# Kernel optimization log

Measured on AMD Instinct MI355X. Metric: run time of the kernel, lower is better.

The kernel has to match this reference:

```python
import jax, jax.numpy as jnp
import numpy as np

H, W = 256, 256
N_PIXELS = H * W
MAX_DIST = float(np.sqrt(H ** 2 + W ** 2))
RESIZED = jnp.array([H, W], dtype=jnp.float32)

# all_img_locations: cartesian product of rows x cols, shape [N_PIXELS, 2] as (row, col)
_rr, _cc = jnp.meshgrid(jnp.arange(H), jnp.arange(W), indexing='ij')
LOCS = jnp.stack([_rr, _cc], axis=-1).reshape(-1, 2).astype(jnp.float32)


def setup_inputs() -> dict:
    key = jax.random.key(0)
    k1, k2, k3 = jax.random.split(key, 3)
    B, M = 8, 128
    # probability map in open interval (0,1) so log(p) and log(1-p) are finite
    prob_map = jnp.clip(jax.random.uniform(k1, (B, H, W), dtype=jnp.float32), 1e-4, 1.0 - 1e-4)
    # gt heatmap: mostly <1 with a sprinkling of exact 1.0 'center' pixels (so pos_count > 0)
    u = jax.random.uniform(k2, (B, H, W), dtype=jnp.float32)
    gt_map = jnp.where(u > 0.999, jnp.float32(1.0), u * 0.999)
    # ground-truth points (row, col) in [0, H) x [0, W)
    gt = jax.random.uniform(k3, (B, M, 2), dtype=jnp.float32) * RESIZED
    # original image sizes (height, width)
    orig_sizes = jnp.ones((B, 2), dtype=jnp.float32) * 1024.0
    return {"prob_map": prob_map, "gt_map": gt_map, "gt": gt, "orig_sizes": orig_sizes}


def _center_focal_loss(pred, g, alpha=2, beta=4):
    pos = (g == 1.0).astype(pred.dtype)
    neg = (g < 1.0).astype(pred.dtype)
    pos_term = (1.0 - pred) ** alpha * jnp.log(pred) * pos
    neg_term = (1.0 - g) ** beta * pred ** alpha * jnp.log1p(-pred) * neg
    return -((pos_term + neg_term).sum() / pos.sum())


def _whd_terms(pm_b, gt_b, orig_size_b):
    norm = orig_size_b / RESIZED                      # [2]
    nx = LOCS * norm                                  # [N, 2]
    ny = gt_b * norm                                  # [M, 2]
    diff = nx[:, None, :] - ny[None, :, :]            # [N, M, 2]
    d = jnp.sqrt(jnp.sum(diff * diff, axis=-1))       # [N, M]
    p = pm_b.reshape(-1)                              # [N]
    n_est = p.sum()
    term1 = jnp.sum(p * d.min(axis=1)) / (n_est + 1e-6)
    weighted = (1.0 - p)[:, None] * MAX_DIST + p[:, None] * d
    term2 = weighted.min(axis=0).mean()               # generalized mean reduces to min over pixels
    return term1, term2


def reference(prob_map, gt_map, gt, orig_sizes):
    terms_1, terms_2 = jax.vmap(_whd_terms)(prob_map, gt, orig_sizes)
    # original loop overwrites terms_3 each iteration -> only last batch element's focal loss survives
    terms_3 = _center_focal_loss(prob_map[-1], gt_map[-1])
    return terms_1.mean() + terms_2.mean() + terms_3
```

## Files before the change

### kernel.cpp

```cpp
#include <hip/hip_runtime.h>
#include <math.h>


#define HH 256
#define WW 256
#define NPIX (HH*WW)
#define MM 128
#define BB 8
#define MAXDIST 362.03867196751236f
#define PBLK 128
#define NBLK (BB*PBLK)
#define TPB 256
#define PXT 2
#define MCH 16
#define NCH (MM/MCH)
#define POISON 0xAAAAAAAAu
#define LASTTOK (POISON + (unsigned)(NBLK - 1))

__device__ __forceinline__ float fast_sqrt(float x) {
  float r;
  asm volatile("v_sqrt_f32 %0, %1" : "=v"(r) : "v"(x));
  return r;
}

__device__ __forceinline__ float wave_sum(float v) {
#pragma unroll
  for (int off = 32; off > 0; off >>= 1) v += __shfl_xor(v, off, 64);
  return v;
}

__global__ __launch_bounds__(TPB, 4) void whd_fused(
    const float* __restrict__ prob, const float* __restrict__ gtmap,
    const float* __restrict__ gt, const float* __restrict__ osz,
    unsigned* __restrict__ colmin,
    float* __restrict__ partials,
    unsigned* __restrict__ counter,
    float* __restrict__ out) {
  const int b   = blockIdx.x >> 7;
  const int blk = blockIdx.x & (PBLK - 1);
  const int tid = threadIdx.x;
  const int lane = tid & 63;

  __shared__ float2 sgt[MM];
  __shared__ float wred[TPB / 64][4];
  __shared__ int lastFlag;
  __shared__ float sT[TPB / 64];
  __shared__ float sA[BB], sC[BB], sF[BB], sG[BB];

  const float ny = osz[b * 2 + 0] * (1.0f / HH);
  const float nx = osz[b * 2 + 1] * (1.0f / WW);

  if (tid < MM) {
    float gy = gt[(b * MM + tid) * 2 + 0] * ny;
    float gx = gt[(b * MM + tid) * 2 + 1] * nx;
    sgt[tid] = make_float2(gy, gx);
  }
  __syncthreads();

  const int pixBase = blk * (NPIX / PBLK) + tid * PXT;
  const float pyf = (float)(pixBase >> 8) * ny;
  const int col0 = pixBase & (WW - 1);

  const float* pp = prob + b * NPIX + pixBase;
  float2 pv = *(const float2*)(pp);
  float p[PXT] = {pv.x, pv.y};

  float pxf[PXT], bb[PXT], md[PXT];
#pragma unroll
  for (int i = 0; i < PXT; i++) {
    pxf[i] = (float)(col0 + i) * nx;
    bb[i]  = (1.0f - p[i]) * MAXDIST;
    md[i]  = 3.0e38f;
  }

#pragma unroll 1
  for (int c = 0; c < NCH; c++) {
    float gx[MCH], dy2[MCH], cm[MCH];
#pragma unroll
    for (int j = 0; j < MCH; j++) {
      float2 g = sgt[c * MCH + j];
      float dy = pyf - g.x;
      dy2[j] = dy * dy;
      gx[j]  = g.y;
      cm[j]  = 3.0e38f;
    }
#pragma unroll
    for (int i = 0; i < PXT; i++) {
      const float pi = p[i], bi = bb[i], xi = pxf[i];
      float mdi = md[i];
#pragma unroll
      for (int j = 0; j < MCH; j++) {
        float dx = xi - gx[j];
        float d  = fast_sqrt(fmaf(dx, dx, dy2[j]));
        mdi   = fminf(mdi, d);
        cm[j] = fminf(cm[j], fmaf(pi, d, bi));
      }
      md[i] = mdi;
    }

    {
      const bool hi5 = (lane & 32) != 0;
#pragma unroll
      for (int k = 0; k < 8; k++) {
        float keep = hi5 ? cm[k + 8] : cm[k];
        float send = hi5 ? cm[k] : cm[k + 8];
        cm[k] = fminf(keep, __shfl_xor(send, 32, 64));
      }
      const bool hi4 = (lane & 16) != 0;
#pragma unroll
      for (int k = 0; k < 4; k++) {
        float keep = hi4 ? cm[k + 4] : cm[k];
        float send = hi4 ? cm[k] : cm[k + 4];
        cm[k] = fminf(keep, __shfl_xor(send, 16, 64));
      }
      const bool hi3 = (lane & 8) != 0;
#pragma unroll
      for (int k = 0; k < 2; k++) {
        float keep = hi3 ? cm[k + 2] : cm[k];
        float send = hi3 ? cm[k] : cm[k + 2];
        cm[k] = fminf(keep, __shfl_xor(send, 8, 64));
      }
      const bool hi2 = (lane & 4) != 0;
      {
        float keep = hi2 ? cm[1] : cm[0];
        float send = hi2 ? cm[0] : cm[1];
        cm[0] = fminf(keep, __shfl_xor(send, 4, 64));
      }
      float v = cm[0];
      v = fminf(v, __shfl_xor(v, 1, 64));
      v = fminf(v, __shfl_xor(v, 2, 64));
      if ((lane & 3) == 0)
        atomicMin(&colmin[b * MM + c * MCH + (lane >> 2)], __float_as_uint(v));
    }
  }

  float spd = 0.0f, sp = 0.0f;
#pragma unroll
  for (int i = 0; i < PXT; i++) {
    spd = fmaf(p[i], md[i], spd);
    sp += p[i];
  }

  float fs = 0.0f, fc = 0.0f;
  if (b == BB - 1) {
    const float* gp = gtmap + b * NPIX + pixBase;
    float2 gv2 = *(const float2*)(gp);
    float gv[PXT] = {gv2.x, gv2.y};
#pragma unroll
    for (int i = 0; i < PXT; i++) {
      float g = gv[i], pi = p[i];
      if (g == 1.0f) {
        float om = 1.0f - pi;
        fs += om * om * logf(pi);
        fc += 1.0f;
      } else {
        float t = 1.0f - g, t2 = t * t;
        fs += t2 * t2 * pi * pi * log1pf(-pi);
      }
    }
  }

  spd = wave_sum(spd);
  sp  = wave_sum(sp);
  fs  = wave_sum(fs);
  fc  = wave_sum(fc);

  const int wid = tid >> 6;
  if (lane == 0) {
    wred[wid][0] = spd; wred[wid][1] = sp; wred[wid][2] = fs; wred[wid][3] = fc;
  }
  __syncthreads();

  if (tid == 0) {
    float a = 0, c2 = 0, e = 0, f = 0;
#pragma unroll
    for (int w = 0; w < TPB / 64; w++) {
      a += wred[w][0]; c2 += wred[w][1]; e += wred[w][2]; f += wred[w][3];
    }
    float* pt = partials + blockIdx.x * 4;
    pt[0] = a; pt[1] = c2; pt[2] = e; pt[3] = f;
    __threadfence();
    unsigned old = atomicAdd(counter, 1u);
    lastFlag = (old == LASTTOK) ? 1 : 0;
  }
  __syncthreads();
  if (lastFlag == 0) return;

  __threadfence();

  float s = 0.0f;
  for (int i = tid; i < BB * MM; i += TPB)
    s += __uint_as_float(atomicAdd(&colmin[i], 0u));
  s = wave_sum(s);
  if (lane == 0) sT[wid] = s;

  const int g = tid >> 5;
  const int i = tid & 31;
  float a = 0, c = 0, e = 0, f = 0;
  for (int k = i; k < PBLK; k += 32) {
    float* pt = partials + (g * PBLK + k) * 4;
    a += atomicAdd(pt + 0, 0.0f);
    c += atomicAdd(pt + 1, 0.0f);
    e += atomicAdd(pt + 2, 0.0f);
    f += atomicAdd(pt + 3, 0.0f);
  }
#pragma unroll
  for (int off = 16; off > 0; off >>= 1) {
    a += __shfl_xor(a, off, 64); c += __shfl_xor(c, off, 64);
    e += __shfl_xor(e, off, 64); f += __shfl_xor(f, off, 64);
  }
  if (i == 0) { sA[g] = a; sC[g] = c; sF[g] = e; sG[g] = f; }
  __syncthreads();

  if (tid == 0) {
    float t2 = (sT[0] + sT[1] + sT[2] + sT[3]) * (1.0f / (BB * MM));
    float t1 = 0.0f;
    for (int b2 = 0; b2 < BB; b2++) t1 += sA[b2] / (sC[b2] + 1e-6f);
    t1 *= (1.0f / BB);
    float fsum = 0.0f, fcnt = 0.0f;
    for (int b2 = 0; b2 < BB; b2++) { fsum += sF[b2]; fcnt += sG[b2]; }
    out[0] = t1 + t2 - fsum / fcnt;
  }
}

extern "C" void kernel_launch(void* const* d_in, const int* in_sizes, int n_in,
                              void* d_out, int out_size, void* d_ws, size_t ws_size,
                              hipStream_t stream) {
  const float* prob  = (const float*)d_in[0];
  const float* gtmap = (const float*)d_in[1];
  const float* gt    = (const float*)d_in[2];
  const float* osz   = (const float*)d_in[3];
  float* out = (float*)d_out;

  unsigned* colmin  = (unsigned*)d_ws;
  float* partials   = (float*)((char*)d_ws + 4096);
  unsigned* counter = (unsigned*)((char*)d_ws + 4096 + NBLK * 16);

  whd_fused<<<NBLK, TPB, 0, stream>>>(prob, gtmap, gt, osz, colmin, partials,
                                      counter, out);
}
```

Measured before the change: 98.93 us.

## Partition GT points across waves and stage pixels through LDS to cut shuffles and atomics

Each wave now owns 32 of the 128 GT points for the whole run and loops over all 512 pixels of the block, which are staged in shared memory. Column minima stay in registers across all pixel groups, so the butterfly shuffle reduction and the atomicMin to global happen once per block instead of once per 16-point chunk. Per-pixel row minima are combined across waves through a shared-memory buffer. The sqrt asm also loses `volatile` so the compiler is free to schedule it. The cost is more registers for the 32-entry arrays, about 10 KB of extra LDS, and an extra barrier.

```diff
diff --git a/kernel.cpp b/kernel.cpp
--- a/kernel.cpp
+++ b/kernel.cpp
@@ -11,15 +11,15 @@
 #define PBLK 128
 #define NBLK (BB*PBLK)
 #define TPB 256
-#define PXT 2
-#define MCH 16
-#define NCH (MM/MCH)
+#define NW 4
+#define MW 32
+#define PIXB 512
 #define POISON 0xAAAAAAAAu
 #define LASTTOK (POISON + (unsigned)(NBLK - 1))
 
 __device__ __forceinline__ float fast_sqrt(float x) {
   float r;
-  asm volatile("v_sqrt_f32 %0, %1" : "=v"(r) : "v"(x));
+  asm("v_sqrt_f32 %0, %1" : "=v"(r) : "v"(x));
   return r;
 }
 
@@ -36,16 +36,20 @@
     float* __restrict__ partials,
     unsigned* __restrict__ counter,
     float* __restrict__ out) {
-  const int b   = blockIdx.x >> 7;
-  const int blk = blockIdx.x & (PBLK - 1);
-  const int tid = threadIdx.x;
+  const int b    = blockIdx.x >> 7;
+  const int blk  = blockIdx.x & (PBLK - 1);
+  const int tid  = threadIdx.x;
   const int lane = tid & 63;
+  const int w    = tid >> 6;
 
   __shared__ float2 sgt[MM];
-  __shared__ float wred[TPB / 64][4];
-  __shared__ int lastFlag;
-  __shared__ float sT[TPB / 64];
-  __shared__ float sA[BB], sC[BB], sF[BB], sG[BB];
+  __shared__ float  sp[PIXB];
+  __shared__ float  mdw[NW * PIXB];
+  __shared__ float  scm[MM];
+  __shared__ float  wred[NW][4];
+  __shared__ int    lastFlag;
+  __shared__ float  sT[NW];
+  __shared__ float  sA[BB], sC[BB], sF[BB], sG[BB];
 
   const float ny = osz[b * 2 + 0] * (1.0f / HH);
   const float nx = osz[b * 2 + 1] * (1.0f / WW);
@@ -55,127 +59,133 @@
     float gx = gt[(b * MM + tid) * 2 + 1] * nx;
     sgt[tid] = make_float2(gy, gx);
   }
-  __syncthreads();
-
-  const int pixBase = blk * (NPIX / PBLK) + tid * PXT;
-  const float pyf = (float)(pixBase >> 8) * ny;
-  const int col0 = pixBase & (WW - 1);
-
-  const float* pp = prob + b * NPIX + pixBase;
-  float2 pv = *(const float2*)(pp);
-  float p[PXT] = {pv.x, pv.y};
-
-  float pxf[PXT], bb[PXT], md[PXT];
-#pragma unroll
-  for (int i = 0; i < PXT; i++) {
-    pxf[i] = (float)(col0 + i) * nx;
-    bb[i]  = (1.0f - p[i]) * MAXDIST;
-    md[i]  = 3.0e38f;
-  }
-
-#pragma unroll 1
-  for (int c = 0; c < NCH; c++) {
-    float gx[MCH], dy2[MCH], cm[MCH];
-#pragma unroll
-    for (int j = 0; j < MCH; j++) {
-      float2 g = sgt[c * MCH + j];
-      float dy = pyf - g.x;
-      dy2[j] = dy * dy;
-      gx[j]  = g.y;
-      cm[j]  = 3.0e38f;
-    }
-#pragma unroll
-    for (int i = 0; i < PXT; i++) {
-      const float pi = p[i], bi = bb[i], xi = pxf[i];
-      float mdi = md[i];
-#pragma unroll
-      for (int j = 0; j < MCH; j++) {
-        float dx = xi - gx[j];
-        float d  = fast_sqrt(fmaf(dx, dx, dy2[j]));
-        mdi   = fminf(mdi, d);
-        cm[j] = fminf(cm[j], fmaf(pi, d, bi));
-      }
-      md[i] = mdi;
-    }
-
-    {
-      const bool hi5 = (lane & 32) != 0;
-#pragma unroll
-      for (int k = 0; k < 8; k++) {
-        float keep = hi5 ? cm[k + 8] : cm[k];
-        float send = hi5 ? cm[k] : cm[k + 8];
-        cm[k] = fminf(keep, __shfl_xor(send, 32, 64));
-      }
-      const bool hi4 = (lane & 16) != 0;
-#pragma unroll
-      for (int k = 0; k < 4; k++) {
-        float keep = hi4 ? cm[k + 4] : cm[k];
-        float send = hi4 ? cm[k] : cm[k + 4];
-        cm[k] = fminf(keep, __shfl_xor(send, 16, 64));
-      }
-      const bool hi3 = (lane & 8) != 0;
-#pragma unroll
-      for (int k = 0; k < 2; k++) {
-        float keep = hi3 ? cm[k + 2] : cm[k];
-        float send = hi3 ? cm[k] : cm[k + 2];
-        cm[k] = fminf(keep, __shfl_xor(send, 8, 64));
-      }
-      const bool hi2 = (lane & 4) != 0;
-      {
-        float keep = hi2 ? cm[1] : cm[0];
-        float send = hi2 ? cm[0] : cm[1];
-        cm[0] = fminf(keep, __shfl_xor(send, 4, 64));
-      }
-      float v = cm[0];
-      v = fminf(v, __shfl_xor(v, 1, 64));
-      v = fminf(v, __shfl_xor(v, 2, 64));
-      if ((lane & 3) == 0)
-        atomicMin(&colmin[b * MM + c * MCH + (lane >> 2)], __float_as_uint(v));
-    }
-  }
-
-  float spd = 0.0f, sp = 0.0f;
-#pragma unroll
-  for (int i = 0; i < PXT; i++) {
-    spd = fmaf(p[i], md[i], spd);
-    sp += p[i];
-  }
-
+
+  const int pixBase = blk * PIXB + tid * 2;
+  const float2 pv = *(const float2*)(prob + b * NPIX + pixBase);
+  const float p0 = pv.x, p1 = pv.y;
+  sp[tid * 2] = p0;
+  sp[tid * 2 + 1] = p1;
+  const float spsum = p0 + p1;
   float fs = 0.0f, fc = 0.0f;
   if (b == BB - 1) {
-    const float* gp = gtmap + b * NPIX + pixBase;
-    float2 gv2 = *(const float2*)(gp);
-    float gv[PXT] = {gv2.x, gv2.y};
-#pragma unroll
-    for (int i = 0; i < PXT; i++) {
-      float g = gv[i], pi = p[i];
-      if (g == 1.0f) {
-        float om = 1.0f - pi;
-        fs += om * om * logf(pi);
-        fc += 1.0f;
-      } else {
-        float t = 1.0f - g, t2 = t * t;
-        fs += t2 * t2 * pi * pi * log1pf(-pi);
+    const float2 gv = *(const float2*)(gtmap + b * NPIX + pixBase);
+    {
+      float g = gv.x, pi = p0;
+      if (g == 1.0f) { float om = 1.0f - pi; fs += om * om * logf(pi); fc += 1.0f; }
+      else { float t = 1.0f - g, t2 = t * t; fs += t2 * t2 * pi * pi * log1pf(-pi); }
+    }
+    {
+      float g = gv.y, pi = p1;
+      if (g == 1.0f) { float om = 1.0f - pi; fs += om * om * logf(pi); fc += 1.0f; }
+      else { float t = 1.0f - g, t2 = t * t; fs += t2 * t2 * pi * pi * log1pf(-pi); }
+    }
+  }
+  __syncthreads();
+
+  const float pyf0 = (float)(2 * blk) * ny;
+  const float pyf1 = (float)(2 * blk + 1) * ny;
+  float gxr[MW], dy2[MW], cm[MW];
+#pragma unroll
+  for (int j = 0; j < MW; j++) {
+    float2 g2 = sgt[w * MW + j];
+    gxr[j] = g2.y;
+    cm[j]  = 3.0e38f;
+    float dy = pyf0 - g2.x;
+    dy2[j] = dy * dy;
+  }
+
+#pragma unroll 1
+  for (int g = 0; g < 8; g++) {
+    if (g == 4) {
+#pragma unroll
+      for (int j = 0; j < MW; j++) {
+        float dy = pyf1 - sgt[w * MW + j].x;
+        dy2[j] = dy * dy;
       }
     }
-  }
+    const float pp = sp[g * 64 + lane];
+    const float bi = (1.0f - pp) * MAXDIST;
+    const float xi = (float)(((g & 3) << 6) + lane) * nx;
+    float md0 = 3.0e38f, md1 = 3.0e38f;
+#pragma unroll
+    for (int j = 0; j < MW; j += 2) {
+      float dx0 = xi - gxr[j];
+      float d0  = fast_sqrt(fmaf(dx0, dx0, dy2[j]));
+      md0   = fminf(md0, d0);
+      cm[j] = fminf(cm[j], fmaf(pp, d0, bi));
+      float dx1 = xi - gxr[j + 1];
+      float d1  = fast_sqrt(fmaf(dx1, dx1, dy2[j + 1]));
+      md1       = fminf(md1, d1);
+      cm[j + 1] = fminf(cm[j + 1], fmaf(pp, d1, bi));
+    }
+    mdw[w * PIXB + g * 64 + lane] = fminf(md0, md1);
+  }
+
+  {
+    const bool h5 = (lane & 32) != 0;
+#pragma unroll
+    for (int k = 0; k < 16; k++) {
+      float keep = h5 ? cm[k + 16] : cm[k];
+      float send = h5 ? cm[k] : cm[k + 16];
+      cm[k] = fminf(keep, __shfl_xor(send, 32, 64));
+    }
+    const bool h4 = (lane & 16) != 0;
+#pragma unroll
+    for (int k = 0; k < 8; k++) {
+      float keep = h4 ? cm[k + 8] : cm[k];
+      float send = h4 ? cm[k] : cm[k + 8];
+      cm[k] = fminf(keep, __shfl_xor(send, 16, 64));
+    }
+    const bool h3 = (lane & 8) != 0;
+#pragma unroll
+    for (int k = 0; k < 4; k++) {
+      float keep = h3 ? cm[k + 4] : cm[k];
+      float send = h3 ? cm[k] : cm[k + 4];
+      cm[k] = fminf(keep, __shfl_xor(send, 8, 64));
+    }
+    const bool h2 = (lane & 4) != 0;
+#pragma unroll
+    for (int k = 0; k < 2; k++) {
+      float keep = h2 ? cm[k + 2] : cm[k];
+      float send = h2 ? cm[k] : cm[k + 2];
+      cm[k] = fminf(keep, __shfl_xor(send, 4, 64));
+    }
+    const bool h1 = (lane & 2) != 0;
+    {
+      float keep = h1 ? cm[1] : cm[0];
+      float send = h1 ? cm[0] : cm[1];
+      cm[0] = fminf(keep, __shfl_xor(send, 2, 64));
+    }
+    float v = fminf(cm[0], __shfl_xor(cm[0], 1, 64));
+    if ((lane & 1) == 0) scm[w * MW + ((lane >> 1) & 31)] = v;
+  }
+  __syncthreads();
+
+  const int px0 = 2 * tid, px1 = 2 * tid + 1;
+  float mdf0 = fminf(fminf(mdw[0 * PIXB + px0], mdw[1 * PIXB + px0]),
+                     fminf(mdw[2 * PIXB + px0], mdw[3 * PIXB + px0]));
+  float mdf1 = fminf(fminf(mdw[0 * PIXB + px1], mdw[1 * PIXB + px1]),
+                     fminf(mdw[2 * PIXB + px1], mdw[3 * PIXB + px1]));
+  float spd = 0.0f;
+  spd = fmaf(p0, mdf0, spd);
+  spd = fmaf(p1, mdf1, spd);
+
+  if (tid < MM) atomicMin(&colmin[b * MM + tid], __float_as_uint(scm[tid]));
 
   spd = wave_sum(spd);
-  sp  = wave_sum(sp);
-  fs  = wave_sum(fs);
-  fc  = wave_sum(fc);
-
-  const int wid = tid >> 6;
+  float spw = wave_sum(spsum);
+  fs = wave_sum(fs);
+  fc = wave_sum(fc);
   if (lane == 0) {
-    wred[wid][0] = spd; wred[wid][1] = sp; wred[wid][2] = fs; wred[wid][3] = fc;
+    wred[w][0] = spd; wred[w][1] = spw; wred[w][2] = fs; wred[w][3] = fc;
   }
   __syncthreads();
 
   if (tid == 0) {
     float a = 0, c2 = 0, e = 0, f = 0;
 #pragma unroll
-    for (int w = 0; w < TPB / 64; w++) {
-      a += wred[w][0]; c2 += wred[w][1]; e += wred[w][2]; f += wred[w][3];
+    for (int wv = 0; wv < NW; wv++) {
+      a += wred[wv][0]; c2 += wred[wv][1]; e += wred[wv][2]; f += wred[wv][3];
     }
     float* pt = partials + blockIdx.x * 4;
     pt[0] = a; pt[1] = c2; pt[2] = e; pt[3] = f;
@@ -192,13 +202,13 @@
   for (int i = tid; i < BB * MM; i += TPB)
     s += __uint_as_float(atomicAdd(&colmin[i], 0u));
   s = wave_sum(s);
-  if (lane == 0) sT[wid] = s;
-
-  const int g = tid >> 5;
-  const int i = tid & 31;
+  if (lane == 0) sT[w] = s;
+
+  const int gb = tid >> 5;
+  const int i  = tid & 31;
   float a = 0, c = 0, e = 0, f = 0;
   for (int k = i; k < PBLK; k += 32) {
-    float* pt = partials + (g * PBLK + k) * 4;
+    float* pt = partials + (gb * PBLK + k) * 4;
     a += atomicAdd(pt + 0, 0.0f);
     c += atomicAdd(pt + 1, 0.0f);
     e += atomicAdd(pt + 2, 0.0f);
@@ -209,7 +219,7 @@
     a += __shfl_xor(a, off, 64); c += __shfl_xor(c, off, 64);
     e += __shfl_xor(e, off, 64); f += __shfl_xor(f, off, 64);
   }
-  if (i == 0) { sA[g] = a; sC[g] = c; sF[g] = e; sG[g] = f; }
+  if (i == 0) { sA[gb] = a; sC[gb] = c; sF[gb] = e; sG[gb] = f; }
   __syncthreads();
 
   if (tid == 0) {
```

Measured after the change: 86.24 us. -12.8%, faster.
